# Performance work log

Hardware: AMD Instinct MI355X
Metric: run time of the kernel (lower is better)

Reference implementation:

```python
import jax, jax.numpy as jnp
import numpy as np

B, N, T, F = 8, 2000, 64, 32
H = 128    # lstm_hidden
GH = 128   # gnn_hidden
E = 32000  # edges


def setup_inputs() -> dict:
    key = jax.random.key(0)
    ks = jax.random.split(key, 12)
    s = 0.05
    return {
        "x": jax.random.normal(ks[0], (B, N, T, F), jnp.float32),
        "edge_index": jax.random.randint(ks[1], (2, E), 0, N, dtype=jnp.int32),
        # LSTM params (torch gate order i, f, g, o)
        "Wih": jax.random.normal(ks[2], (4 * H, F), jnp.float32) * s,
        "Whh": jax.random.normal(ks[3], (4 * H, H), jnp.float32) * s,
        "bih": jax.random.normal(ks[4], (4 * H,), jnp.float32) * s,
        "bhh": jax.random.normal(ks[5], (4 * H,), jnp.float32) * s,
        # GCNConv params
        "gcn_W": jax.random.normal(ks[6], (H, GH), jnp.float32) * s,
        "gcn_b": jax.random.normal(ks[7], (GH,), jnp.float32) * s,
        # shared MLP head
        "mlp_W1": jax.random.normal(ks[8], (GH, GH // 2), jnp.float32) * s,
        "mlp_b1": jax.random.normal(ks[9], (GH // 2,), jnp.float32) * s,
        "mlp_W2": jax.random.normal(ks[10], (GH // 2, 1), jnp.float32) * s,
        "mlp_b2": jax.random.normal(ks[11], (1,), jnp.float32) * s,
    }


def _lstm_last_h(x, Wih, Whh, bih, bhh):
    # x: [M, T, F] -> last hidden state [M, H]
    M = x.shape[0]
    xg = jnp.einsum('mtf,gf->mtg', x, Wih) + bih  # precompute input gates [M, T, 4H]

    def step(carry, xg_t):
        h, c = carry
        z = xg_t + h @ Whh.T + bhh
        i, f, g, o = jnp.split(z, 4, axis=-1)
        i = jax.nn.sigmoid(i)
        f = jax.nn.sigmoid(f)
        g = jnp.tanh(g)
        o = jax.nn.sigmoid(o)
        c = f * c + i * g
        h = o * jnp.tanh(c)
        return (h, c), None

    h0 = jnp.zeros((M, H), x.dtype)
    c0 = jnp.zeros((M, H), x.dtype)
    (h, _), _ = jax.lax.scan(step, (h0, c0), jnp.swapaxes(xg, 0, 1))
    return h


def reference(x, edge_index, Wih, Whh, bih, bhh, gcn_W, gcn_b,
              mlp_W1, mlp_b1, mlp_W2, mlp_b2):
    Bx, Nx, Tx, Fx = x.shape
    # LSTM over all B*N node sequences, take last hidden state
    h = _lstm_last_h(x.reshape(Bx * Nx, Tx, Fx), Wih, Whh, bih, bhh)
    node_features = h.reshape(Bx, Nx, H)

    # GCNConv (PyG semantics): add self-loops, symmetric normalization
    loops = jnp.arange(Nx, dtype=edge_index.dtype)
    src = jnp.concatenate([edge_index[0], loops])
    dst = jnp.concatenate([edge_index[1], loops])
    deg = jnp.zeros((Nx,), x.dtype).at[dst].add(1.0)
    dinv = jnp.where(deg > 0, jax.lax.rsqrt(deg), 0.0)
    norm = dinv[src] * dinv[dst]  # [E+N]

    xw = node_features @ gcn_W                     # [B, N, GH]
    msgs = xw[:, src, :] * norm[None, :, None]     # gather + scale [B, E+N, GH]
    agg = jnp.zeros((Bx, Nx, GH), x.dtype).at[:, dst, :].add(msgs) + gcn_b

    # shared MLP head (dropout is identity in eval mode)
    h1 = jax.nn.silu(agg @ mlp_W1 + mlp_b1)
    out = h1 @ mlp_W2 + mlp_b2                     # [B, N, 1]
    return out.squeeze(-1)                         # [B, N]
```

## Files before the change

### kernel.cpp

```cpp
#include <hip/hip_runtime.h>

typedef _Float16 f16x8 __attribute__((ext_vector_type(8)));
typedef _Float16 f16x4 __attribute__((ext_vector_type(4)));
typedef _Float16 f16x2 __attribute__((ext_vector_type(2)));
typedef float f32x4 __attribute__((ext_vector_type(4)));

#define NB_   8
#define NN_   2000
#define TT_   64
#define FF_   32
#define HH_   128
#define EE_   32000
#define KD    160
#define RSTR  192
#define NODES 64

__device__ __forceinline__ float fexp2(float v) { return __builtin_amdgcn_exp2f(v); }
__device__ __forceinline__ float frcp(float v)  { return __builtin_amdgcn_rcpf(v); }

__global__ void prep_kernel(const float* __restrict__ Wih, const float* __restrict__ Whh,
                            const float* __restrict__ bih, const float* __restrict__ bhh,
                            const float* __restrict__ gcnW,
                            _Float16* __restrict__ W16, _Float16* __restrict__ Wg16,
                            float* __restrict__ bias, float* __restrict__ deg) {
  int idx = blockIdx.x * 256 + threadIdx.x;
  if (idx < 512 * KD) {
    int col = idx / KD, k = idx % KD;
    float v = (k < 32) ? Wih[col * 32 + k] : Whh[col * 128 + (k - 32)];
    float sc = (col >= 256 && col < 384) ? -2.88539008f : -1.44269504f;
    W16[idx] = (_Float16)(v * sc);
  } else if (idx < 512 * KD + 128 * 128) {
    int i2 = idx - 512 * KD;
    int colg = i2 >> 7, k = i2 & 127;
    Wg16[i2] = (_Float16)gcnW[k * 128 + colg];
  } else if (idx < 512 * KD + 128 * 128 + 512) {
    int i3 = idx - (512 * KD + 128 * 128);
    float sc = (i3 >= 256 && i3 < 384) ? -2.88539008f : -1.44269504f;
    bias[i3] = (bih[i3] + bhh[i3]) * sc;
  } else if (idx < 512 * KD + 128 * 128 + 512 + NN_) {
    deg[idx - (512 * KD + 128 * 128 + 512)] = 0.f;
  }
}

__global__ void deg_kernel(const int* __restrict__ ei, float* __restrict__ deg) {
  int e = blockIdx.x * 256 + threadIdx.x;
  if (e < EE_ + NN_) {
    int d = (e < EE_) ? ei[EE_ + e] : (e - EE_);
    atomicAdd(&deg[d], 1.f);
  }
}

__global__ void scan_kernel(const float* __restrict__ deg, int* __restrict__ offs,
                            int* __restrict__ cursor, float* __restrict__ dinv) {
  __shared__ int s0[2048], s1[2048];
  int t = threadIdx.x;
  for (int i = t; i < 2048; i += 1024) s0[i] = (i < NN_) ? ((int)deg[i] - 1) : 0;
  __syncthreads();
  int* src = s0; int* dst = s1;
  for (int off = 1; off < 2048; off <<= 1) {
    for (int i = t; i < 2048; i += 1024)
      dst[i] = src[i] + ((i >= off) ? src[i - off] : 0);
    __syncthreads();
    int* tmp = src; src = dst; dst = tmp;
  }
  for (int i = t; i < NN_; i += 1024) {
    int exc = src[i] - ((int)deg[i] - 1);
    offs[i] = exc;
    cursor[i] = exc;
    float d = deg[i];
    dinv[i] = (d > 0.f) ? __builtin_amdgcn_rsqf(d) : 0.f;
  }
}

__global__ void fill_kernel(const int* __restrict__ ei, const float* __restrict__ dinv,
                            int* __restrict__ cursor, int* __restrict__ csr_src,
                            float* __restrict__ csr_w) {
  int e = blockIdx.x * 256 + threadIdx.x;
  if (e >= EE_) return;
  int s = ei[e], d = ei[EE_ + e];
  int pos = atomicAdd(&cursor[d], 1);
  csr_src[pos] = s;
  csr_w[pos] = dinv[s] * dinv[d];
}

__global__ __launch_bounds__(512, 2) void lstm_gcn_kernel(
    const float* __restrict__ x, const _Float16* __restrict__ W16,
    const float* __restrict__ bias, const _Float16* __restrict__ Wg16,
    _Float16* __restrict__ xwT) {
  __shared__ _Float16 A[NODES * RSTR];
  const int tid  = threadIdx.x;
  const int wave = tid >> 6;
  const int lane = tid & 63;
  const int n15  = lane & 15;
  const int q    = lane >> 4;
  const int m    = n15 & 7;
  const int hm   = m >> 2;
  const int qx   = q ^ (m & 3);
  const int node0 = blockIdx.x * NODES;

  f16x8 Af[4][4];
  f16x8 Ax[4];
  f32x4 Bz[4];
#pragma unroll
  for (int g = 0; g < 4; ++g) {
    const int row = g * 128 + wave * 16 + n15;
#pragma unroll
    for (int kc = 1; kc < 5; ++kc)
      Af[g][kc - 1] = *(const f16x8*)(W16 + row * KD + kc * 32 + q * 8);
    Ax[g] = *(const f16x8*)(W16 + row * KD + q * 8);
    Bz[g] = *(const f32x4*)(bias + g * 128 + wave * 16 + q * 4);
  }

  const int bRow = n15 * RSTR + (qx << 3);
  const int hOff = n15 * RSTR + (((4 + 2 * wave + (q >> 1)) ^ m) << 3) + ((q & 1) << 2);

  const int xrow = tid >> 3;
  const int xf   = (tid & 7) * 4;
  const int xOff = xrow * RSTR + (((xf >> 3) ^ (xrow & 7)) << 3) + (xf & 7);
  const float* xb = x + (size_t)(node0 + xrow) * (TT_ * FF_) + xf;

#pragma unroll
  for (int j = 0; j < 2; ++j) {
    int idx = tid * 2 + j;
    int row = idx >> 4, ci = idx & 15;
    f16x8 z8 = {(_Float16)0, (_Float16)0, (_Float16)0, (_Float16)0,
                (_Float16)0, (_Float16)0, (_Float16)0, (_Float16)0};
    *(f16x8*)(A + row * RSTR + (((4 + ci) ^ (row & 7)) << 3)) = z8;
  }
  {
    float4 v = *(const float4*)xb;
    f16x4 p = {(_Float16)v.x, (_Float16)v.y, (_Float16)v.z, (_Float16)v.w};
    *(f16x4*)(A + xOff) = p;
  }
  __syncthreads();

  f32x4 acc[4][4], c[4];
#pragma unroll
  for (int nt = 0; nt < 4; ++nt) c[nt] = (f32x4){0, 0, 0, 0};

  for (int t = 0; t < TT_; ++t) {
    {
#pragma unroll
      for (int nt = 0; nt < 4; ++nt)
#pragma unroll
        for (int g = 0; g < 4; ++g) acc[nt][g] = Bz[g];
      __builtin_amdgcn_s_setprio(1);
#pragma unroll
      for (int nt = 0; nt < 4; ++nt) {
        f16x8 bf = *(const f16x8*)(A + nt * (16 * RSTR) + bRow + (hm << 5));
#pragma unroll
        for (int g = 0; g < 4; ++g)
          acc[nt][g] = __builtin_amdgcn_mfma_f32_16x16x32_f16(Ax[g], bf, acc[nt][g], 0, 0, 0);
      }
#pragma unroll
      for (int kc = 1; kc < 5; ++kc)
#pragma unroll
        for (int nt = 0; nt < 4; ++nt) {
          f16x8 bf = *(const f16x8*)(A + nt * (16 * RSTR) + bRow + ((kc ^ hm) << 5));
#pragma unroll
          for (int g = 0; g < 4; ++g)
            acc[nt][g] = __builtin_amdgcn_mfma_f32_16x16x32_f16(Af[g][kc - 1], bf, acc[nt][g], 0, 0, 0);
        }
      __builtin_amdgcn_s_setprio(0);
    }
    const bool more = (t + 1 < TT_);
    float4 xv;
    if (more) xv = *(const float4*)(xb + (t + 1) * FF_);
    __syncthreads();

#pragma unroll
    for (int nt = 0; nt < 4; ++nt) {
      f16x4 hp;
#pragma unroll
      for (int r = 0; r < 4; ++r) {
        float Ei = fexp2(acc[nt][0][r]);
        float Ef = fexp2(acc[nt][1][r]);
        float Eg = fexp2(acc[nt][2][r]);
        float Eo = fexp2(acc[nt][3][r]);
        float ai = 1.f + Ei, af = 1.f + Ef, ag = 1.f + Eg, ao = 1.f + Eo;
        float pig = ai * ag;
        float num = c[nt][r] * pig + (1.f - Eg) * af;
        float cn  = num * frcp(af * pig);
        c[nt][r] = cn;
        float Ec = fexp2(-2.88539008f * cn);
        float hn = (1.f - Ec) * frcp((1.f + Ec) * ao);
        hp[r] = (_Float16)hn;
      }
      *(f16x4*)(A + nt * (16 * RSTR) + hOff) = hp;
    }
    if (more) {
      f16x4 p = {(_Float16)xv.x, (_Float16)xv.y, (_Float16)xv.z, (_Float16)xv.w};
      *(f16x4*)(A + xOff) = p;
    }
    __syncthreads();
  }

  f16x8 Ag[4];
#pragma unroll
  for (int kc = 0; kc < 4; ++kc)
    Ag[kc] = *(const f16x8*)(Wg16 + (wave * 16 + n15) * HH_ + kc * 32 + q * 8);
  f32x4 acc2[4];
#pragma unroll
  for (int nt = 0; nt < 4; ++nt) acc2[nt] = (f32x4){0, 0, 0, 0};
  __builtin_amdgcn_s_setprio(1);
#pragma unroll
  for (int kc = 0; kc < 4; ++kc)
#pragma unroll
    for (int nt = 0; nt < 4; ++nt) {
      f16x8 bf = *(const f16x8*)(A + nt * (16 * RSTR) + bRow + (((kc + 1) ^ hm) << 5));
      acc2[nt] = __builtin_amdgcn_mfma_f32_16x16x32_f16(Ag[kc], bf, acc2[nt], 0, 0, 0);
    }
  __builtin_amdgcn_s_setprio(0);
#pragma unroll
  for (int nt = 0; nt < 4; ++nt) {
    int mnode = node0 + nt * 16 + n15;
    int b = mnode / NN_;
    int n = mnode - b * NN_;
    f16x4 hv = {(_Float16)acc2[nt][0], (_Float16)acc2[nt][1],
                (_Float16)acc2[nt][2], (_Float16)acc2[nt][3]};
    *(f16x4*)(xwT + ((size_t)n * 8 + b) * HH_ + wave * 16 + q * 4) = hv;
  }
}

__global__ __launch_bounds__(256) void gathermlp_kernel(
    const _Float16* __restrict__ xwT, const int* __restrict__ offs,
    const float* __restrict__ deg, const float* __restrict__ dinv,
    const int* __restrict__ csr_src, const float* __restrict__ csr_w,
    const float* __restrict__ gcnb,
    const float* __restrict__ W1, const float* __restrict__ b1,
    const float* __restrict__ W2, const float* __restrict__ b2,
    float* __restrict__ out) {
  __shared__ float aggs[8][128];
  __shared__ float W1T[64][132];
  const int d = blockIdx.x;
  const int tid = threadIdx.x;
  for (int i = tid; i < 8192; i += 256) {
    int k = i >> 6, j = i & 63;
    W1T[j][k] = W1[i];
  }
  {
    const int b    = tid >> 5;
    const int dcol = (tid & 31) * 4;
    const int boff = b * 128 + dcol;
    const int beg = offs[d];
    const int cnt = (int)deg[d] - 1;
    float a0 = 0.f, a1 = 0.f, a2 = 0.f, a3 = 0.f;
    int e = 0;
    for (; e + 3 < cnt; e += 4) {
      int s0 = csr_src[beg + e],     s1 = csr_src[beg + e + 1];
      int s2 = csr_src[beg + e + 2], s3 = csr_src[beg + e + 3];
      float w0 = csr_w[beg + e],     w1 = csr_w[beg + e + 1];
      float w2 = csr_w[beg + e + 2], w3 = csr_w[beg + e + 3];
      f16x4 v0 = *(const f16x4*)(xwT + (size_t)s0 * 1024 + boff);
      f16x4 v1 = *(const f16x4*)(xwT + (size_t)s1 * 1024 + boff);
      f16x4 v2 = *(const f16x4*)(xwT + (size_t)s2 * 1024 + boff);
      f16x4 v3 = *(const f16x4*)(xwT + (size_t)s3 * 1024 + boff);
      a0 += w0 * (float)v0[0] + w1 * (float)v1[0] + w2 * (float)v2[0] + w3 * (float)v3[0];
      a1 += w0 * (float)v0[1] + w1 * (float)v1[1] + w2 * (float)v2[1] + w3 * (float)v3[1];
      a2 += w0 * (float)v0[2] + w1 * (float)v1[2] + w2 * (float)v2[2] + w3 * (float)v3[2];
      a3 += w0 * (float)v0[3] + w1 * (float)v1[3] + w2 * (float)v2[3] + w3 * (float)v3[3];
    }
    for (; e < cnt; ++e) {
      int s = csr_src[beg + e];
      float w = csr_w[beg + e];
      f16x4 v = *(const f16x4*)(xwT + (size_t)s * 1024 + boff);
      a0 += w * (float)v[0]; a1 += w * (float)v[1];
      a2 += w * (float)v[2]; a3 += w * (float)v[3];
    }
    {
      float di = dinv[d];
      float w = di * di;
      f16x4 v = *(const f16x4*)(xwT + (size_t)d * 1024 + boff);
      a0 += w * (float)v[0]; a1 += w * (float)v[1];
      a2 += w * (float)v[2]; a3 += w * (float)v[3];
    }
    float4 bj = *(const float4*)(gcnb + dcol);
    *(float4*)&aggs[b][dcol] = (float4){a0 + bj.x, a1 + bj.y, a2 + bj.z, a3 + bj.w};
  }
  __syncthreads();
  const int b = tid >> 5;
  const int t = tid & 31;
  float acc1 = b1[t], acc2 = b1[t + 32];
#pragma unroll 8
  for (int kc = 0; kc < 32; ++kc) {
    float4 a  = *(const float4*)&aggs[b][kc * 4];
    float4 w1 = *(const float4*)&W1T[t][kc * 4];
    float4 w2 = *(const float4*)&W1T[t + 32][kc * 4];
    acc1 += a.x * w1.x + a.y * w1.y + a.z * w1.z + a.w * w1.w;
    acc2 += a.x * w2.x + a.y * w2.y + a.z * w2.z + a.w * w2.w;
  }
  float s1 = acc1 * frcp(1.f + fexp2(-1.44269504f * acc1));
  float s2 = acc2 * frcp(1.f + fexp2(-1.44269504f * acc2));
  float part = s1 * W2[t] + s2 * W2[t + 32];
#pragma unroll
  for (int msk = 16; msk >= 1; msk >>= 1) part += __shfl_xor(part, msk);
  if (t == 0) out[(size_t)b * NN_ + d] = part + b2[0];
}

extern "C" void kernel_launch(void* const* d_in, const int* in_sizes, int n_in,
                              void* d_out, int out_size, void* d_ws, size_t ws_size,
                              hipStream_t stream) {
  const float* x    = (const float*)d_in[0];
  const int*   ei   = (const int*)d_in[1];
  const float* Wih  = (const float*)d_in[2];
  const float* Whh  = (const float*)d_in[3];
  const float* bih  = (const float*)d_in[4];
  const float* bhh  = (const float*)d_in[5];
  const float* gcnW = (const float*)d_in[6];
  const float* gcnb = (const float*)d_in[7];
  const float* W1   = (const float*)d_in[8];
  const float* b1   = (const float*)d_in[9];
  const float* W2   = (const float*)d_in[10];
  const float* b2   = (const float*)d_in[11];
  float* out = (float*)d_out;
  char* ws = (char*)d_ws;

  _Float16* W16    = (_Float16*)(ws);
  _Float16* Wg16   = (_Float16*)(ws + 163840);
  float*    bias   = (float*)(ws + 196608);
  _Float16* xwT    = (_Float16*)(ws + 198656);
  float*    deg    = (float*)(ws + 8390656);
  float*    dinv   = (float*)(ws + 8398848);
  int*      offs   = (int*)(ws + 8407040);
  int*      cursor = (int*)(ws + 8415232);
  int*      csrs   = (int*)(ws + 8423424);
  float*    csrw   = (float*)(ws + 8551424);

  prep_kernel<<<394, 256, 0, stream>>>(Wih, Whh, bih, bhh, gcnW, W16, Wg16, bias, deg);
  deg_kernel<<<133, 256, 0, stream>>>(ei, deg);
  scan_kernel<<<1, 1024, 0, stream>>>(deg, offs, cursor, dinv);
  fill_kernel<<<125, 256, 0, stream>>>(ei, dinv, cursor, csrs, csrw);
  lstm_gcn_kernel<<<250, 512, 0, stream>>>(x, W16, bias, Wg16, xwT);
  gathermlp_kernel<<<NN_, 256, 0, stream>>>(xwT, offs, deg, dinv, csrs, csrw,
                                            gcnb, W1, b1, W2, b2, out);
}
```

Before: 376.3 us.

## Fuse weight prep and CSR graph construction into a single setup kernel

Merges the four preprocessing launches (weight conversion, degree histogram, scan, CSR fill) into one kernel. Most blocks convert weights, while one extra block builds the degree histogram, prefix scan and CSR fill using shared-memory atomics. This removes three launches and the global atomics/round trips between them. In exchange the graph build runs serially in a single block of 512 threads, which may sit on the critical path ahead of the LSTM kernel.

```diff
diff --git a/kernel.cpp b/kernel.cpp
--- a/kernel.cpp
+++ b/kernel.cpp
@@ -18,69 +18,67 @@
 __device__ __forceinline__ float fexp2(float v) { return __builtin_amdgcn_exp2f(v); }
 __device__ __forceinline__ float frcp(float v)  { return __builtin_amdgcn_rcpf(v); }
 
-__global__ void prep_kernel(const float* __restrict__ Wih, const float* __restrict__ Whh,
-                            const float* __restrict__ bih, const float* __restrict__ bhh,
-                            const float* __restrict__ gcnW,
-                            _Float16* __restrict__ W16, _Float16* __restrict__ Wg16,
-                            float* __restrict__ bias, float* __restrict__ deg) {
-  int idx = blockIdx.x * 256 + threadIdx.x;
-  if (idx < 512 * KD) {
-    int col = idx / KD, k = idx % KD;
-    float v = (k < 32) ? Wih[col * 32 + k] : Whh[col * 128 + (k - 32)];
-    float sc = (col >= 256 && col < 384) ? -2.88539008f : -1.44269504f;
-    W16[idx] = (_Float16)(v * sc);
-  } else if (idx < 512 * KD + 128 * 128) {
-    int i2 = idx - 512 * KD;
-    int colg = i2 >> 7, k = i2 & 127;
-    Wg16[i2] = (_Float16)gcnW[k * 128 + colg];
-  } else if (idx < 512 * KD + 128 * 128 + 512) {
-    int i3 = idx - (512 * KD + 128 * 128);
-    float sc = (i3 >= 256 && i3 < 384) ? -2.88539008f : -1.44269504f;
-    bias[i3] = (bih[i3] + bhh[i3]) * sc;
-  } else if (idx < 512 * KD + 128 * 128 + 512 + NN_) {
-    deg[idx - (512 * KD + 128 * 128 + 512)] = 0.f;
-  }
-}
-
-__global__ void deg_kernel(const int* __restrict__ ei, float* __restrict__ deg) {
-  int e = blockIdx.x * 256 + threadIdx.x;
-  if (e < EE_ + NN_) {
-    int d = (e < EE_) ? ei[EE_ + e] : (e - EE_);
-    atomicAdd(&deg[d], 1.f);
-  }
-}
-
-__global__ void scan_kernel(const float* __restrict__ deg, int* __restrict__ offs,
-                            int* __restrict__ cursor, float* __restrict__ dinv) {
+__global__ __launch_bounds__(512) void setup_kernel(
+    const float* __restrict__ Wih, const float* __restrict__ Whh,
+    const float* __restrict__ bih, const float* __restrict__ bhh,
+    const float* __restrict__ gcnW, const int* __restrict__ ei,
+    _Float16* __restrict__ W16, _Float16* __restrict__ Wg16,
+    float* __restrict__ bias,
+    int* __restrict__ offs, float* __restrict__ deg, float* __restrict__ dinv,
+    int* __restrict__ csr_src, float* __restrict__ csr_w) {
+  if (blockIdx.x < 193) {
+    int idx = blockIdx.x * 512 + threadIdx.x;
+    if (idx < 512 * KD) {
+      int col = idx / KD, k = idx % KD;
+      float v = (k < 32) ? Wih[col * 32 + k] : Whh[col * 128 + (k - 32)];
+      float sc = (col >= 256 && col < 384) ? -2.88539008f : -1.44269504f;
+      W16[idx] = (_Float16)(v * sc);
+    } else if (idx < 512 * KD + 128 * 128) {
+      int i2 = idx - 512 * KD;
+      int colg = i2 >> 7, k = i2 & 127;
+      Wg16[i2] = (_Float16)gcnW[k * 128 + colg];
+    } else if (idx < 512 * KD + 128 * 128 + 512) {
+      int i3 = idx - (512 * KD + 128 * 128);
+      float sc = (i3 >= 256 && i3 < 384) ? -2.88539008f : -1.44269504f;
+      bias[i3] = (bih[i3] + bhh[i3]) * sc;
+    }
+    return;
+  }
+  __shared__ int hist[2048];
   __shared__ int s0[2048], s1[2048];
-  int t = threadIdx.x;
-  for (int i = t; i < 2048; i += 1024) s0[i] = (i < NN_) ? ((int)deg[i] - 1) : 0;
+  __shared__ float dinvL[2048];
+  const int t = threadIdx.x;
+  for (int i = t; i < 2048; i += 512) hist[i] = (i < NN_) ? 1 : 0;
+  __syncthreads();
+  for (int e = t; e < EE_; e += 512) atomicAdd(&hist[ei[EE_ + e]], 1);
+  __syncthreads();
+  for (int i = t; i < 2048; i += 512) s0[i] = (i < NN_) ? (hist[i] - 1) : 0;
   __syncthreads();
   int* src = s0; int* dst = s1;
   for (int off = 1; off < 2048; off <<= 1) {
-    for (int i = t; i < 2048; i += 1024)
+    for (int i = t; i < 2048; i += 512)
       dst[i] = src[i] + ((i >= off) ? src[i - off] : 0);
     __syncthreads();
     int* tmp = src; src = dst; dst = tmp;
   }
-  for (int i = t; i < NN_; i += 1024) {
-    int exc = src[i] - ((int)deg[i] - 1);
+  int* cur = dst;
+  for (int i = t; i < NN_; i += 512) {
+    int dgi = hist[i];
+    int exc = src[i] - (dgi - 1);
     offs[i] = exc;
-    cursor[i] = exc;
-    float d = deg[i];
-    dinv[i] = (d > 0.f) ? __builtin_amdgcn_rsqf(d) : 0.f;
-  }
-}
-
-__global__ void fill_kernel(const int* __restrict__ ei, const float* __restrict__ dinv,
-                            int* __restrict__ cursor, int* __restrict__ csr_src,
-                            float* __restrict__ csr_w) {
-  int e = blockIdx.x * 256 + threadIdx.x;
-  if (e >= EE_) return;
-  int s = ei[e], d = ei[EE_ + e];
-  int pos = atomicAdd(&cursor[d], 1);
-  csr_src[pos] = s;
-  csr_w[pos] = dinv[s] * dinv[d];
+    cur[i] = exc;
+    deg[i] = (float)dgi;
+    float dv = __builtin_amdgcn_rsqf((float)dgi);
+    dinvL[i] = dv;
+    dinv[i] = dv;
+  }
+  __syncthreads();
+  for (int e = t; e < EE_; e += 512) {
+    int s = ei[e], d = ei[EE_ + e];
+    int pos = atomicAdd(&cur[d], 1);
+    csr_src[pos] = s;
+    csr_w[pos] = dinvL[s] * dinvL[d];
+  }
 }
 
 __global__ __launch_bounds__(512, 2) void lstm_gcn_kernel(
@@ -322,14 +320,11 @@
   float*    deg    = (float*)(ws + 8390656);
   float*    dinv   = (float*)(ws + 8398848);
   int*      offs   = (int*)(ws + 8407040);
-  int*      cursor = (int*)(ws + 8415232);
   int*      csrs   = (int*)(ws + 8423424);
   float*    csrw   = (float*)(ws + 8551424);
 
-  prep_kernel<<<394, 256, 0, stream>>>(Wih, Whh, bih, bhh, gcnW, W16, Wg16, bias, deg);
-  deg_kernel<<<133, 256, 0, stream>>>(ei, deg);
-  scan_kernel<<<1, 1024, 0, stream>>>(deg, offs, cursor, dinv);
-  fill_kernel<<<125, 256, 0, stream>>>(ei, dinv, cursor, csrs, csrw);
+  setup_kernel<<<194, 512, 0, stream>>>(Wih, Whh, bih, bhh, gcnW, ei,
+                                        W16, Wg16, bias, offs, deg, dinv, csrs, csrw);
   lstm_gcn_kernel<<<250, 512, 0, stream>>>(x, W16, bias, Wg16, xwT);
   gathermlp_kernel<<<NN_, 256, 0, stream>>>(xwT, offs, deg, dinv, csrs, csrw,
                                             gcnb, W1, b1, W2, b2, out);
```

After: 465.2 us. 1.24x slower.
